# Kernel tuning notes

Hardware: AMD Instinct MI355X
Metric: run time of the kernel (lower is better)

## Reference

```python
import jax, jax.numpy as jnp
import numpy as np

B, L, C, D = 4, 2048, 64, 4


def setup_inputs() -> dict:
    key = jax.random.key(0)
    k1, k2, k3, k4 = jax.random.split(key, 4)
    # |A| kept < ~0.92 so the length-2048 recurrence stays bounded
    A_re = jax.random.uniform(k1, (B, L, C, D), jnp.float32, -0.65, 0.65)
    A_im = jax.random.uniform(k2, (B, L, C, D), jnp.float32, -0.65, 0.65)
    X_re = jax.random.normal(k3, (B, L, C, D, D), jnp.float32)
    X_im = jax.random.normal(k4, (B, L, C, D, D), jnp.float32)
    return {"A_re": A_re, "A_im": A_im, "X_re": X_re, "X_im": X_im}


def _combine(c1, c2):
    # first-order linear recurrence combine: (a, x) o (b, y) = (b*a, b*x + y)
    a1, x1 = c1
    a2, x2 = c2
    return a2 * a1, a2 * x1 + x2


def reference(A_re, A_im, X_re, X_im):
    # Diagonal complex pscan: Y[t] = A[t] * Y[t-1] + X[t], elementwise,
    # with diagonal A [B,L,C,D] broadcast over the trailing D dim of X [B,L,C,D,D]
    A = (A_re + 1j * A_im).astype(jnp.complex64)[..., None]  # [B,L,C,D,1]
    X = (X_re + 1j * X_im).astype(jnp.complex64)             # [B,L,C,D,D]
    _, Y = jax.lax.associative_scan(_combine, (A, X), axis=1)
    # return real view [B,L,C,D,D,2] (real, imag) like torch.view_as_real
    return jnp.stack([Y.real, Y.imag], axis=-1)
```

## Files before the change

### kernel.cpp

```cpp
#include <hip/hip_runtime.h>

#define BB 4
#define LL 2048
#define KK 256


template<int G, int LOGG>
__global__ __launch_bounds__(256) void pscan_phase1(
    const float* __restrict__ A_re, const float* __restrict__ A_im,
    const float4* __restrict__ X4_re, const float4* __restrict__ X4_im,
    float2* __restrict__ agg_p, float4* __restrict__ agg_s) {
  constexpr int T = LL / G;
  int u  = blockIdx.x * 256 + threadIdx.x;
  int k  = u & (KK - 1);
  int bg = u >> 8;
  int g  = bg & (G - 1);
  int b  = bg >> LOGG;
  int t0 = g * T;
  long base = (long)(b * LL + t0) * KK + k;

  float p_re = 1.f, p_im = 0.f;
  float s_re[4] = {0.f, 0.f, 0.f, 0.f};
  float s_im[4] = {0.f, 0.f, 0.f, 0.f};
#pragma unroll 8
  for (int t = 0; t < T; ++t) {
    long idx = base + (long)t * KK;
    float are = A_re[idx], aim = A_im[idx];
    float4 xr = X4_re[idx], xi = X4_im[idx];
    float xrv[4] = {xr.x, xr.y, xr.z, xr.w};
    float xiv[4] = {xi.x, xi.y, xi.z, xi.w};
#pragma unroll
    for (int j = 0; j < 4; ++j) {
      float nr = fmaf(are, s_re[j], fmaf(-aim, s_im[j], xrv[j]));
      float ni = fmaf(are, s_im[j], fmaf( aim, s_re[j], xiv[j]));
      s_re[j] = nr; s_im[j] = ni;
    }
    float npr = are * p_re - aim * p_im;
    float npi = are * p_im + aim * p_re;
    p_re = npr; p_im = npi;
  }
  agg_p[u]       = make_float2(p_re, p_im);
  agg_s[2*u]     = make_float4(s_re[0], s_im[0], s_re[1], s_im[1]);
  agg_s[2*u + 1] = make_float4(s_re[2], s_im[2], s_re[3], s_im[3]);
}

template<int G, int LOGG>
__global__ __launch_bounds__(256) void pscan_phase2(
    const float2* __restrict__ agg_p, float4* __restrict__ agg_s) {
  int u = blockIdx.x * 256 + threadIdx.x;
  int g = u & (G - 1);
  int chain = u >> LOGG;
  int b = chain >> 8;
  int k = chain & (KK - 1);
  long idx = (long)(b * G + g) * KK + k;

  float2 p  = agg_p[idx];
  float4 s01 = agg_s[2*idx], s23 = agg_s[2*idx + 1];
  float pr = p.x, pi = p.y;
  float sr[4] = {s01.x, s01.z, s23.x, s23.z};
  float si[4] = {s01.y, s01.w, s23.y, s23.w};

#pragma unroll
  for (int d = 1; d < G; d <<= 1) {
    float plr = __shfl_up(pr, d, 64);
    float pli = __shfl_up(pi, d, 64);
    float slr[4], sli[4];
#pragma unroll
    for (int j = 0; j < 4; ++j) {
      slr[j] = __shfl_up(sr[j], d, 64);
      sli[j] = __shfl_up(si[j], d, 64);
    }
    if (g >= d) {
#pragma unroll
      for (int j = 0; j < 4; ++j) {
        float nr = fmaf(pr, slr[j], fmaf(-pi, sli[j], sr[j]));
        float ni = fmaf(pr, sli[j], fmaf( pi, slr[j], si[j]));
        sr[j] = nr; si[j] = ni;
      }
      float npr = pr * plr - pi * pli;
      float npi = pr * pli + pi * plr;
      pr = npr; pi = npi;
    }
  }
  float er[4], ei[4];
#pragma unroll
  for (int j = 0; j < 4; ++j) {
    er[j] = __shfl_up(sr[j], 1, 64);
    ei[j] = __shfl_up(si[j], 1, 64);
  }
  if (g == 0) {
#pragma unroll
    for (int j = 0; j < 4; ++j) { er[j] = 0.f; ei[j] = 0.f; }
  }
  agg_s[2*idx]     = make_float4(er[0], ei[0], er[1], ei[1]);
  agg_s[2*idx + 1] = make_float4(er[2], ei[2], er[3], ei[3]);
}

template<int G, int LOGG>
__global__ __launch_bounds__(256) void pscan_phase3(
    const float* __restrict__ A_re, const float* __restrict__ A_im,
    const float4* __restrict__ X4_re, const float4* __restrict__ X4_im,
    const float4* __restrict__ agg_s, float4* __restrict__ out4) {
  constexpr int T = LL / G;
  int u  = blockIdx.x * 256 + threadIdx.x;
  int k  = u & (KK - 1);
  int bg = u >> 8;
  int g  = bg & (G - 1);
  int b  = bg >> LOGG;
  int t0 = g * T;
  long base = (long)(b * LL + t0) * KK + k;

  float4 c01 = agg_s[2*u], c23 = agg_s[2*u + 1];
  float yr[4] = {c01.x, c01.z, c23.x, c23.z};
  float yi[4] = {c01.y, c01.w, c23.y, c23.w};
#pragma unroll 8
  for (int t = 0; t < T; ++t) {
    long idx = base + (long)t * KK;
    float are = A_re[idx], aim = A_im[idx];
    float4 xr = X4_re[idx], xi = X4_im[idx];
    float xrv[4] = {xr.x, xr.y, xr.z, xr.w};
    float xiv[4] = {xi.x, xi.y, xi.z, xi.w};
#pragma unroll
    for (int j = 0; j < 4; ++j) {
      float nr = fmaf(are, yr[j], fmaf(-aim, yi[j], xrv[j]));
      float ni = fmaf(are, yi[j], fmaf( aim, yr[j], xiv[j]));
      yr[j] = nr; yi[j] = ni;
    }
    out4[2*idx]     = make_float4(yr[0], yi[0], yr[1], yi[1]);
    out4[2*idx + 1] = make_float4(yr[2], yi[2], yr[3], yi[3]);
  }
}

template<int G, int LOGG>
static void launch_all(const float* A_re, const float* A_im,
                       const float4* X4_re, const float4* X4_im,
                       void* d_ws, float4* out4, hipStream_t stream) {
  float2* agg_p = (float2*)d_ws;
  float4* agg_s = (float4*)((char*)d_ws + (size_t)BB * G * KK * sizeof(float2));
  int blocks = BB * G;
  pscan_phase1<G, LOGG><<<blocks, 256, 0, stream>>>(A_re, A_im, X4_re, X4_im, agg_p, agg_s);
  pscan_phase2<G, LOGG><<<blocks, 256, 0, stream>>>(agg_p, agg_s);
  pscan_phase3<G, LOGG><<<blocks, 256, 0, stream>>>(A_re, A_im, X4_re, X4_im, agg_s, out4);
}

extern "C" void kernel_launch(void* const* d_in, const int* in_sizes, int n_in,
                              void* d_out, int out_size, void* d_ws, size_t ws_size,
                              hipStream_t stream) {
  const float*  A_re  = (const float*)d_in[0];
  const float*  A_im  = (const float*)d_in[1];
  const float4* X4_re = (const float4*)d_in[2];
  const float4* X4_im = (const float4*)d_in[3];
  float4* out4 = (float4*)d_out;

  const size_t need64 = (size_t)BB * 64 * KK * (sizeof(float2) + 2 * sizeof(float4));
  if (ws_size >= need64) {
    launch_all<64, 6>(A_re, A_im, X4_re, X4_im, d_ws, out4, stream);
  } else {
    launch_all<32, 5>(A_re, A_im, X4_re, X4_im, d_ws, out4, stream);
  }
}
```

Before: 155.4 us.

## Increase chunk count to 256 and make phase 2 a sequential per-chain carry scan

```diff
diff --git a/kernel.cpp b/kernel.cpp
--- a/kernel.cpp
+++ b/kernel.cpp
@@ -6,7 +6,7 @@
 
 
 template<int G, int LOGG>
-__global__ __launch_bounds__(256) void pscan_phase1(
+__global__ __launch_bounds__(256, 4) void pscan_phase1(
     const float* __restrict__ A_re, const float* __restrict__ A_im,
     const float4* __restrict__ X4_re, const float4* __restrict__ X4_im,
     float2* __restrict__ agg_p, float4* __restrict__ agg_s) {
@@ -16,13 +16,12 @@
   int bg = u >> 8;
   int g  = bg & (G - 1);
   int b  = bg >> LOGG;
-  int t0 = g * T;
-  long base = (long)(b * LL + t0) * KK + k;
+  long base = (long)(b * LL + g * T) * KK + k;
 
   float p_re = 1.f, p_im = 0.f;
   float s_re[4] = {0.f, 0.f, 0.f, 0.f};
   float s_im[4] = {0.f, 0.f, 0.f, 0.f};
-#pragma unroll 8
+#pragma unroll
   for (int t = 0; t < T; ++t) {
     long idx = base + (long)t * KK;
     float are = A_re[idx], aim = A_im[idx];
@@ -44,60 +43,35 @@
   agg_s[2*u + 1] = make_float4(s_re[2], s_im[2], s_re[3], s_im[3]);
 }
 
-template<int G, int LOGG>
+template<int G>
 __global__ __launch_bounds__(256) void pscan_phase2(
     const float2* __restrict__ agg_p, float4* __restrict__ agg_s) {
   int u = blockIdx.x * 256 + threadIdx.x;
-  int g = u & (G - 1);
-  int chain = u >> LOGG;
-  int b = chain >> 8;
-  int k = chain & (KK - 1);
-  long idx = (long)(b * G + g) * KK + k;
-
-  float2 p  = agg_p[idx];
-  float4 s01 = agg_s[2*idx], s23 = agg_s[2*idx + 1];
-  float pr = p.x, pi = p.y;
-  float sr[4] = {s01.x, s01.z, s23.x, s23.z};
-  float si[4] = {s01.y, s01.w, s23.y, s23.w};
-
-#pragma unroll
-  for (int d = 1; d < G; d <<= 1) {
-    float plr = __shfl_up(pr, d, 64);
-    float pli = __shfl_up(pi, d, 64);
-    float slr[4], sli[4];
+  int k = u & (KK - 1);
+  int b = u >> 8;
+  float rs_re[4] = {0.f, 0.f, 0.f, 0.f};
+  float rs_im[4] = {0.f, 0.f, 0.f, 0.f};
+#pragma unroll 4
+  for (int g = 0; g < G; ++g) {
+    long idx = (long)(b * G + g) * KK + k;
+    float2 p   = agg_p[idx];
+    float4 s01 = agg_s[2*idx];
+    float4 s23 = agg_s[2*idx + 1];
+    agg_s[2*idx]     = make_float4(rs_re[0], rs_im[0], rs_re[1], rs_im[1]);
+    agg_s[2*idx + 1] = make_float4(rs_re[2], rs_im[2], rs_re[3], rs_im[3]);
+    float svr[4] = {s01.x, s01.z, s23.x, s23.z};
+    float svi[4] = {s01.y, s01.w, s23.y, s23.w};
 #pragma unroll
     for (int j = 0; j < 4; ++j) {
-      slr[j] = __shfl_up(sr[j], d, 64);
-      sli[j] = __shfl_up(si[j], d, 64);
-    }
-    if (g >= d) {
-#pragma unroll
-      for (int j = 0; j < 4; ++j) {
-        float nr = fmaf(pr, slr[j], fmaf(-pi, sli[j], sr[j]));
-        float ni = fmaf(pr, sli[j], fmaf( pi, slr[j], si[j]));
-        sr[j] = nr; si[j] = ni;
-      }
-      float npr = pr * plr - pi * pli;
-      float npi = pr * pli + pi * plr;
-      pr = npr; pi = npi;
+      float nr = fmaf(p.x, rs_re[j], fmaf(-p.y, rs_im[j], svr[j]));
+      float ni = fmaf(p.x, rs_im[j], fmaf( p.y, rs_re[j], svi[j]));
+      rs_re[j] = nr; rs_im[j] = ni;
     }
   }
-  float er[4], ei[4];
-#pragma unroll
-  for (int j = 0; j < 4; ++j) {
-    er[j] = __shfl_up(sr[j], 1, 64);
-    ei[j] = __shfl_up(si[j], 1, 64);
-  }
-  if (g == 0) {
-#pragma unroll
-    for (int j = 0; j < 4; ++j) { er[j] = 0.f; ei[j] = 0.f; }
-  }
-  agg_s[2*idx]     = make_float4(er[0], ei[0], er[1], ei[1]);
-  agg_s[2*idx + 1] = make_float4(er[2], ei[2], er[3], ei[3]);
 }
 
 template<int G, int LOGG>
-__global__ __launch_bounds__(256) void pscan_phase3(
+__global__ __launch_bounds__(256, 4) void pscan_phase3(
     const float* __restrict__ A_re, const float* __restrict__ A_im,
     const float4* __restrict__ X4_re, const float4* __restrict__ X4_im,
     const float4* __restrict__ agg_s, float4* __restrict__ out4) {
@@ -107,13 +81,12 @@
   int bg = u >> 8;
   int g  = bg & (G - 1);
   int b  = bg >> LOGG;
-  int t0 = g * T;
-  long base = (long)(b * LL + t0) * KK + k;
+  long base = (long)(b * LL + g * T) * KK + k;
 
   float4 c01 = agg_s[2*u], c23 = agg_s[2*u + 1];
   float yr[4] = {c01.x, c01.z, c23.x, c23.z};
   float yi[4] = {c01.y, c01.w, c23.y, c23.w};
-#pragma unroll 8
+#pragma unroll
   for (int t = 0; t < T; ++t) {
     long idx = base + (long)t * KK;
     float are = A_re[idx], aim = A_im[idx];
@@ -139,7 +112,7 @@
   float4* agg_s = (float4*)((char*)d_ws + (size_t)BB * G * KK * sizeof(float2));
   int blocks = BB * G;
   pscan_phase1<G, LOGG><<<blocks, 256, 0, stream>>>(A_re, A_im, X4_re, X4_im, agg_p, agg_s);
-  pscan_phase2<G, LOGG><<<blocks, 256, 0, stream>>>(agg_p, agg_s);
+  pscan_phase2<G><<<(BB * KK) / 256, 256, 0, stream>>>(agg_p, agg_s);
   pscan_phase3<G, LOGG><<<blocks, 256, 0, stream>>>(A_re, A_im, X4_re, X4_im, agg_s, out4);
 }
 
@@ -152,10 +125,10 @@
   const float4* X4_im = (const float4*)d_in[3];
   float4* out4 = (float4*)d_out;
 
-  const size_t need64 = (size_t)BB * 64 * KK * (sizeof(float2) + 2 * sizeof(float4));
-  if (ws_size >= need64) {
+  const size_t need256 = (size_t)BB * 256 * KK * (sizeof(float2) + 2 * sizeof(float4));
+  if (ws_size >= need256) {
+    launch_all<256, 8>(A_re, A_im, X4_re, X4_im, d_ws, out4, stream);
+  } else {
     launch_all<64, 6>(A_re, A_im, X4_re, X4_im, d_ws, out4, stream);
-  } else {
-    launch_all<32, 5>(A_re, A_im, X4_re, X4_im, d_ws, out4, stream);
   }
 }
```

Measured after the change: 214.9 us. 38.3% more time.

## Split scan into 256 chunks with block-level two-tier carry scan and nontemporal stores

Applied to the files above, without the earlier changes.

```diff
diff --git a/kernel.cpp b/kernel.cpp
--- a/kernel.cpp
+++ b/kernel.cpp
@@ -3,27 +3,28 @@
 #define BB 4
 #define LL 2048
 #define KK 256
+#define GG 256
+#define TT (LL / GG)
+
+typedef float nfloat4 __attribute__((ext_vector_type(4)));
 
 
-template<int G, int LOGG>
-__global__ __launch_bounds__(256) void pscan_phase1(
+__global__ __launch_bounds__(256, 4) void pscan_phase1(
     const float* __restrict__ A_re, const float* __restrict__ A_im,
     const float4* __restrict__ X4_re, const float4* __restrict__ X4_im,
     float2* __restrict__ agg_p, float4* __restrict__ agg_s) {
-  constexpr int T = LL / G;
   int u  = blockIdx.x * 256 + threadIdx.x;
   int k  = u & (KK - 1);
   int bg = u >> 8;
-  int g  = bg & (G - 1);
-  int b  = bg >> LOGG;
-  int t0 = g * T;
-  long base = (long)(b * LL + t0) * KK + k;
+  int g  = bg & (GG - 1);
+  int b  = bg >> 8;
+  long base = (long)(b * LL + g * TT) * KK + k;
 
   float p_re = 1.f, p_im = 0.f;
   float s_re[4] = {0.f, 0.f, 0.f, 0.f};
   float s_im[4] = {0.f, 0.f, 0.f, 0.f};
-#pragma unroll 8
-  for (int t = 0; t < T; ++t) {
+#pragma unroll
+  for (int t = 0; t < TT; ++t) {
     long idx = base + (long)t * KK;
     float are = A_re[idx], aim = A_im[idx];
     float4 xr = X4_re[idx], xi = X4_im[idx];
@@ -44,24 +45,24 @@
   agg_s[2*u + 1] = make_float4(s_re[2], s_im[2], s_re[3], s_im[3]);
 }
 
-template<int G, int LOGG>
 __global__ __launch_bounds__(256) void pscan_phase2(
     const float2* __restrict__ agg_p, float4* __restrict__ agg_s) {
-  int u = blockIdx.x * 256 + threadIdx.x;
-  int g = u & (G - 1);
-  int chain = u >> LOGG;
-  int b = chain >> 8;
-  int k = chain & (KK - 1);
-  long idx = (long)(b * G + g) * KK + k;
+  __shared__ float lds_p[4][2];
+  __shared__ float lds_s[4][8];
+  int chain = blockIdx.x;
+  int b = chain >> 8, k = chain & (KK - 1);
+  int g = threadIdx.x;
+  int w = g >> 6, l = g & 63;
+  long idx = (long)(b * GG + g) * KK + k;
 
-  float2 p  = agg_p[idx];
+  float2 p   = agg_p[idx];
   float4 s01 = agg_s[2*idx], s23 = agg_s[2*idx + 1];
   float pr = p.x, pi = p.y;
   float sr[4] = {s01.x, s01.z, s23.x, s23.z};
   float si[4] = {s01.y, s01.w, s23.y, s23.w};
 
 #pragma unroll
-  for (int d = 1; d < G; d <<= 1) {
+  for (int d = 1; d < 64; d <<= 1) {
     float plr = __shfl_up(pr, d, 64);
     float pli = __shfl_up(pi, d, 64);
     float slr[4], sli[4];
@@ -70,7 +71,7 @@
       slr[j] = __shfl_up(sr[j], d, 64);
       sli[j] = __shfl_up(si[j], d, 64);
     }
-    if (g >= d) {
+    if (l >= d) {
 #pragma unroll
       for (int j = 0; j < 4; ++j) {
         float nr = fmaf(pr, slr[j], fmaf(-pi, sli[j], sr[j]));
@@ -82,39 +83,69 @@
       pr = npr; pi = npi;
     }
   }
-  float er[4], ei[4];
+
+  float epr = __shfl_up(pr, 1, 64), epi = __shfl_up(pi, 1, 64);
+  float esr[4], esi[4];
 #pragma unroll
   for (int j = 0; j < 4; ++j) {
-    er[j] = __shfl_up(sr[j], 1, 64);
-    ei[j] = __shfl_up(si[j], 1, 64);
+    esr[j] = __shfl_up(sr[j], 1, 64);
+    esi[j] = __shfl_up(si[j], 1, 64);
   }
-  if (g == 0) {
+  if (l == 0) {
+    epr = 1.f; epi = 0.f;
 #pragma unroll
-    for (int j = 0; j < 4; ++j) { er[j] = 0.f; ei[j] = 0.f; }
+    for (int j = 0; j < 4; ++j) { esr[j] = 0.f; esi[j] = 0.f; }
   }
-  agg_s[2*idx]     = make_float4(er[0], ei[0], er[1], ei[1]);
-  agg_s[2*idx + 1] = make_float4(er[2], ei[2], er[3], ei[3]);
+
+  if (l == 63) {
+    lds_p[w][0] = pr; lds_p[w][1] = pi;
+#pragma unroll
+    for (int j = 0; j < 4; ++j) { lds_s[w][2*j] = sr[j]; lds_s[w][2*j+1] = si[j]; }
+  }
+  __syncthreads();
+
+  float wpr = 1.f, wpi = 0.f;
+  float wsr[4] = {0.f,0.f,0.f,0.f}, wsi[4] = {0.f,0.f,0.f,0.f};
+  for (int ww = 0; ww < w; ++ww) {
+    float tpr = lds_p[ww][0], tpi = lds_p[ww][1];
+#pragma unroll
+    for (int j = 0; j < 4; ++j) {
+      float tsr = lds_s[ww][2*j], tsi = lds_s[ww][2*j+1];
+      float nr = fmaf(tpr, wsr[j], fmaf(-tpi, wsi[j], tsr));
+      float ni = fmaf(tpr, wsi[j], fmaf( tpi, wsr[j], tsi));
+      wsr[j] = nr; wsi[j] = ni;
+    }
+    float npr = tpr * wpr - tpi * wpi;
+    float npi = tpr * wpi + tpi * wpr;
+    wpr = npr; wpi = npi;
+  }
+
+  float seedr[4], seedi[4];
+#pragma unroll
+  for (int j = 0; j < 4; ++j) {
+    seedr[j] = fmaf(epr, wsr[j], fmaf(-epi, wsi[j], esr[j]));
+    seedi[j] = fmaf(epr, wsi[j], fmaf( epi, wsr[j], esi[j]));
+  }
+  agg_s[2*idx]     = make_float4(seedr[0], seedi[0], seedr[1], seedi[1]);
+  agg_s[2*idx + 1] = make_float4(seedr[2], seedi[2], seedr[3], seedi[3]);
 }
 
-template<int G, int LOGG>
-__global__ __launch_bounds__(256) void pscan_phase3(
+__global__ __launch_bounds__(256, 4) void pscan_phase3(
     const float* __restrict__ A_re, const float* __restrict__ A_im,
     const float4* __restrict__ X4_re, const float4* __restrict__ X4_im,
-    const float4* __restrict__ agg_s, float4* __restrict__ out4) {
-  constexpr int T = LL / G;
+    const float4* __restrict__ agg_s, nfloat4* __restrict__ out4) {
   int u  = blockIdx.x * 256 + threadIdx.x;
   int k  = u & (KK - 1);
   int bg = u >> 8;
-  int g  = bg & (G - 1);
-  int b  = bg >> LOGG;
-  int t0 = g * T;
-  long base = (long)(b * LL + t0) * KK + k;
+  int g  = bg & (GG - 1);
+  int b  = bg >> 8;
+  long base = (long)(b * LL + g * TT) * KK + k;
 
   float4 c01 = agg_s[2*u], c23 = agg_s[2*u + 1];
   float yr[4] = {c01.x, c01.z, c23.x, c23.z};
   float yi[4] = {c01.y, c01.w, c23.y, c23.w};
-#pragma unroll 8
-  for (int t = 0; t < T; ++t) {
+#pragma unroll
+  for (int t = 0; t < TT; ++t) {
     long idx = base + (long)t * KK;
     float are = A_re[idx], aim = A_im[idx];
     float4 xr = X4_re[idx], xi = X4_im[idx];
@@ -126,21 +157,11 @@
       float ni = fmaf(are, yi[j], fmaf( aim, yr[j], xiv[j]));
       yr[j] = nr; yi[j] = ni;
     }
-    out4[2*idx]     = make_float4(yr[0], yi[0], yr[1], yi[1]);
-    out4[2*idx + 1] = make_float4(yr[2], yi[2], yr[3], yi[3]);
+    nfloat4 o0 = {yr[0], yi[0], yr[1], yi[1]};
+    nfloat4 o1 = {yr[2], yi[2], yr[3], yi[3]};
+    __builtin_nontemporal_store(o0, &out4[2*idx]);
+    __builtin_nontemporal_store(o1, &out4[2*idx + 1]);
   }
-}
-
-template<int G, int LOGG>
-static void launch_all(const float* A_re, const float* A_im,
-                       const float4* X4_re, const float4* X4_im,
-                       void* d_ws, float4* out4, hipStream_t stream) {
-  float2* agg_p = (float2*)d_ws;
-  float4* agg_s = (float4*)((char*)d_ws + (size_t)BB * G * KK * sizeof(float2));
-  int blocks = BB * G;
-  pscan_phase1<G, LOGG><<<blocks, 256, 0, stream>>>(A_re, A_im, X4_re, X4_im, agg_p, agg_s);
-  pscan_phase2<G, LOGG><<<blocks, 256, 0, stream>>>(agg_p, agg_s);
-  pscan_phase3<G, LOGG><<<blocks, 256, 0, stream>>>(A_re, A_im, X4_re, X4_im, agg_s, out4);
 }
 
 extern "C" void kernel_launch(void* const* d_in, const int* in_sizes, int n_in,
@@ -150,12 +171,13 @@
   const float*  A_im  = (const float*)d_in[1];
   const float4* X4_re = (const float4*)d_in[2];
   const float4* X4_im = (const float4*)d_in[3];
-  float4* out4 = (float4*)d_out;
+  nfloat4* out4 = (nfloat4*)d_out;
 
-  const size_t need64 = (size_t)BB * 64 * KK * (sizeof(float2) + 2 * sizeof(float4));
-  if (ws_size >= need64) {
-    launch_all<64, 6>(A_re, A_im, X4_re, X4_im, d_ws, out4, stream);
-  } else {
-    launch_all<32, 5>(A_re, A_im, X4_re, X4_im, d_ws, out4, stream);
-  }
+  float2* agg_p = (float2*)d_ws;
+  float4* agg_s = (float4*)((char*)d_ws + (size_t)BB * GG * KK * sizeof(float2));
+
+  const int blocks = BB * GG;
+  pscan_phase1<<<blocks, 256, 0, stream>>>(A_re, A_im, X4_re, X4_im, agg_p, agg_s);
+  pscan_phase2<<<BB * KK, 256, 0, stream>>>(agg_p, agg_s);
+  pscan_phase3<<<blocks, 256, 0, stream>>>(A_re, A_im, X4_re, X4_im, agg_s, out4);
 }
```

After: 172.1 us. 1.11x slower.
